# Optimization experiments

Measured on AMD Instinct MI355X. Metric: run time of the kernel, lower is better.

The kernel has to match this reference:

```python
import jax, jax.numpy as jnp
import numpy as np

TEMPERATURE = 0.5
BATCH = 2048  # N = batch_size * world_size (world_size = 1)
FEAT = 128
EPS = 1e-8  # torch CosineSimilarity default eps


def _build_mask_indices(N):
    """Replicates mask_correlated_samples + the row-major boolean gather
    sim[mask].reshape(2N, -1). Returns static flat indices [2N, 2N-1]."""
    sub = np.ones((2 * N, 2 * N), dtype=bool)
    np.fill_diagonal(sub, False)
    idx = np.arange(N)
    sub[idx, N + idx] = False
    sub[N + idx, idx] = False
    mask = np.zeros((3 * N, 3 * N), dtype=bool)
    mask[:2 * N, :2 * N] = sub
    mask[idx, 2 * N + idx] = True
    mask[2 * N + idx, idx] = True
    flat = np.nonzero(mask.ravel())[0]  # row-major order, 2N*(2N-1) entries
    return flat.reshape(2 * N, 2 * N - 1)


_NEG_IDX = jnp.asarray(_build_mask_indices(BATCH), dtype=jnp.int32)


def setup_inputs() -> dict:
    key = jax.random.key(0)
    ka, kp, kn = jax.random.split(key, 3)
    return {
        "anchor": jax.random.normal(ka, (BATCH, FEAT), dtype=jnp.float32),
        "pos": jax.random.normal(kp, (BATCH, FEAT), dtype=jnp.float32),
        "neg": jax.random.normal(kn, (BATCH, FEAT), dtype=jnp.float32),
    }


def reference(anchor, pos, neg):
    N = anchor.shape[0]
    z = jnp.concatenate([anchor, pos, neg], axis=0)  # [3N, d]
    zn = z / jnp.maximum(jnp.linalg.norm(z, axis=1, keepdims=True), EPS)
    sim = (zn @ zn.T) / TEMPERATURE  # [3N, 3N]
    # positive pairs: diagonals at offset +/-2N (anchor<->neg pairs)
    sim_i_j = jnp.diagonal(sim, offset=2 * N)[:N]
    sim_j_i = jnp.diagonal(sim, offset=-2 * N)[:N]
    positive = jnp.concatenate([sim_i_j, sim_j_i]).reshape(2 * N, 1)
    # masked gather of negatives (static index table, row-major order)
    negative = jnp.take(sim.ravel(), _NEG_IDX)  # [2N, 2N-1]
    logits = jnp.concatenate([positive, negative], axis=1)  # [2N, 2N]
    # cross-entropy with label 0, reduction='sum', then / (2N)
    loss = jnp.sum(jax.nn.logsumexp(logits, axis=1) - logits[:, 0]) / (2 * N)
    return loss
```

## Files before the change

### kernel.cpp

```cpp
#include <hip/hip_runtime.h>
#include <hip/hip_bf16.h>

#define N_      2048
#define TWO_N   4096
#define DFEAT   128
#define SCALE   2.0f
#define BROWS   128
#define BCOLS   128
#define NT      (BCOLS / 16)
#define LDSTR   136

typedef __attribute__((ext_vector_type(8))) short bf16x8;
typedef __attribute__((ext_vector_type(4))) float f32x4;

__global__ __launch_bounds__(256) void k_prep(const float* __restrict__ a,
                                              const float* __restrict__ p,
                                              const float* __restrict__ ng,
                                              __hip_bfloat16* __restrict__ zn16,
                                              float* __restrict__ dvec,
                                              float* __restrict__ accS,
                                              float* __restrict__ accP) {
  const int wave = threadIdx.x >> 6;
  const int lane = threadIdx.x & 63;
  const int row  = blockIdx.x * 4 + wave;

  if (threadIdx.x < 4)        accS[blockIdx.x * 4 + threadIdx.x] = 0.0f;
  else if (threadIdx.x < 6)   accP[blockIdx.x * 2 + threadIdx.x - 4] = 0.0f;

  if (row < N_) {
    float2 u = ((const float2*)(a  + (size_t)row * DFEAT))[lane];
    float2 w = ((const float2*)(ng + (size_t)row * DFEAT))[lane];
    float saa = u.x * u.x + u.y * u.y;
    float snn = w.x * w.x + w.y * w.y;
    float san = u.x * w.x + u.y * w.y;
#pragma unroll
    for (int m = 1; m < 64; m <<= 1) {
      saa += __shfl_xor(saa, m);
      snn += __shfl_xor(snn, m);
      san += __shfl_xor(san, m);
    }
    float na = fmaxf(sqrtf(saa), 1e-8f);
    float rn = 1.0f / na;
    __hip_bfloat162 h;
    h.x = __float2bfloat16(u.x * rn);
    h.y = __float2bfloat16(u.y * rn);
    ((__hip_bfloat162*)zn16)[row * (DFEAT / 2) + lane] = h;
    if (lane == 0)
      dvec[row] = SCALE * san / (na * fmaxf(sqrtf(snn), 1e-8f));
  } else {
    float2 v = ((const float2*)(p + (size_t)(row - N_) * DFEAT))[lane];
    float ss = v.x * v.x + v.y * v.y;
#pragma unroll
    for (int m = 1; m < 64; m <<= 1) ss += __shfl_xor(ss, m);
    float rn = 1.0f / fmaxf(sqrtf(ss), 1e-8f);
    __hip_bfloat162 h;
    h.x = __float2bfloat16(v.x * rn);
    h.y = __float2bfloat16(v.y * rn);
    ((__hip_bfloat162*)zn16)[row * (DFEAT / 2) + lane] = h;
  }
}

__global__ __launch_bounds__(256) void k_simsum(const __hip_bfloat16* __restrict__ zn16,
                                                float* __restrict__ accS,
                                                float* __restrict__ accP) {
  __shared__ short Bp[BCOLS * LDSTR];

  const int wave = threadIdx.x >> 6;
  const int lane = threadIdx.x & 63;
  const int lr   = lane & 15;
  const int kg   = lane >> 4;
  const int rows_base = blockIdx.x * BROWS + wave * 32;
  const int cb0 = blockIdx.y * BCOLS;
  const short* zs = (const short*)zn16;

  bf16x8 a0[4], a1[4];
#pragma unroll
  for (int kk = 0; kk < 4; ++kk) {
    a0[kk] = *(const bf16x8*)(zs + (size_t)(rows_base + lr) * DFEAT + kk * 32 + kg * 8);
    a1[kk] = *(const bf16x8*)(zs + (size_t)(rows_base + 16 + lr) * DFEAT + kk * 32 + kg * 8);
  }

#pragma unroll
  for (int it = 0; it < 8; ++it) {
    const int g   = it * 256 + threadIdx.x;
    const int col = g >> 4;
    const int q   = g & 15;
    bf16x8 v = *(const bf16x8*)(zs + (size_t)(cb0 + col) * DFEAT + q * 8);
    *(bf16x8*)(&Bp[col * LDSTR + q * 8]) = v;
  }
  __syncthreads();

  const bool hi = (rows_base >= N_);
  int rrow[2][4], prt[2][4];
#pragma unroll
  for (int t = 0; t < 2; ++t)
#pragma unroll
    for (int j = 0; j < 4; ++j) {
      rrow[t][j] = rows_base + t * 16 + kg * 4 + j;
      prt[t][j]  = hi ? (rrow[t][j] - N_) : (rrow[t][j] + N_);
    }

  float accPv[2][4] = {{0.f,0.f,0.f,0.f},{0.f,0.f,0.f,0.f}};
  float accSv[2][4] = {{0.f,0.f,0.f,0.f},{0.f,0.f,0.f,0.f}};

#pragma unroll 1
  for (int ct = 0; ct < NT; ++ct) {
    bf16x8 b[4];
#pragma unroll
    for (int kk = 0; kk < 4; ++kk)
      b[kk] = *(const bf16x8*)(&Bp[(ct * 16 + lr) * LDSTR + kk * 32 + kg * 8]);

    f32x4 acc0 = {0.f, 0.f, 0.f, 0.f};
    f32x4 acc1 = {0.f, 0.f, 0.f, 0.f};
#pragma unroll
    for (int kk = 0; kk < 4; ++kk) {
      acc0 = __builtin_amdgcn_mfma_f32_16x16x32_bf16(a0[kk], b[kk], acc0, 0, 0, 0);
      acc1 = __builtin_amdgcn_mfma_f32_16x16x32_bf16(a1[kk], b[kk], acc1, 0, 0, 0);
    }

    const int c = cb0 + ct * 16 + lr;
#pragma unroll
    for (int j = 0; j < 4; ++j) {
      {
        float e = __expf(SCALE * acc0[j]);
        const bool excl = (c == rrow[0][j]) || (c == prt[0][j]);
        e = excl ? 0.0f : e;
        if (hi) {
          const bool toP = (c < prt[0][j]);
          accPv[0][j] += toP ? e : 0.0f;
          accSv[0][j] += toP ? 0.0f : e;
        } else {
          accSv[0][j] += e;
        }
      }
      {
        float e = __expf(SCALE * acc1[j]);
        const bool excl = (c == rrow[1][j]) || (c == prt[1][j]);
        e = excl ? 0.0f : e;
        if (hi) {
          const bool toP = (c < prt[1][j]);
          accPv[1][j] += toP ? e : 0.0f;
          accSv[1][j] += toP ? 0.0f : e;
        } else {
          accSv[1][j] += e;
        }
      }
    }
  }

#pragma unroll
  for (int t = 0; t < 2; ++t)
#pragma unroll
    for (int j = 0; j < 4; ++j) {
      float pv = accPv[t][j], sv = accSv[t][j];
#pragma unroll
      for (int m = 1; m < 16; m <<= 1) {
        sv += __shfl_xor(sv, m);
        if (hi) pv += __shfl_xor(pv, m);
      }
      if (lr == 0) {
        atomicAdd(&accS[rrow[t][j]], sv);
        if (hi) atomicAdd(&accP[rrow[t][j] - N_], pv);
      }
    }
}

__global__ __launch_bounds__(1024) void k_final(const float* __restrict__ dvec,
                                                const float* __restrict__ accS,
                                                const float* __restrict__ accP,
                                                float* __restrict__ out) {
  __shared__ float Elds[N_];
  __shared__ float red[16];
  const int tid = threadIdx.x;
  float dpart = 0.f;
  for (int i = tid; i < N_; i += 1024) {
    float E = __expf(dvec[i]);
    Elds[i] = E;
    dpart += E;
  }
#pragma unroll
  for (int m = 1; m < 64; m <<= 1) dpart += __shfl_xor(dpart, m);
  const int w = tid >> 6, l = tid & 63;
  if (l == 0) red[w] = dpart;
  __syncthreads();
  float Dsum = 0.f;
#pragma unroll
  for (int k = 0; k < 16; ++k) Dsum += red[k];
  __syncthreads();

  float part = 0.f;
  for (int r = tid; r < TWO_N; r += 1024) {
    float S = accS[r];
    float t;
    if (r < N_) {
      t = logf(2.0f * Elds[r] + S) - dvec[r];
    } else {
      const int i = r - N_;
      const float extra = (i < N_ - 1) ? accP[i + 1] : Dsum;
      t = logf(Elds[i] + S + extra) - dvec[i];
    }
    part += t;
  }
#pragma unroll
  for (int m = 1; m < 64; m <<= 1) part += __shfl_xor(part, m);
  if (l == 0) red[w] = part;
  __syncthreads();
  if (tid == 0) {
    float tot = 0.f;
#pragma unroll
    for (int k = 0; k < 16; ++k) tot += red[k];
    out[0] = tot / (float)TWO_N;
  }
}

extern "C" void kernel_launch(void* const* d_in, const int* in_sizes, int n_in,
                              void* d_out, int out_size, void* d_ws, size_t ws_size,
                              hipStream_t stream) {
  const float* a  = (const float*)d_in[0];
  const float* p  = (const float*)d_in[1];
  const float* ng = (const float*)d_in[2];

  char* ws = (char*)d_ws;
  __hip_bfloat16* zn16 = (__hip_bfloat16*)ws;
  float* dvec = (float*)(ws + (size_t)TWO_N * DFEAT * 2);
  float* accS = dvec + TWO_N;
  float* accP = accS + TWO_N;

  k_prep<<<TWO_N / 4, 256, 0, stream>>>(a, p, ng, zn16, dvec, accS, accP);
  k_simsum<<<dim3(TWO_N / BROWS, TWO_N / BCOLS), 256, 0, stream>>>(zn16, accS, accP);
  k_final<<<1, 1024, 0, stream>>>(dvec, accS, accP, (float*)d_out);
}
```

Before: 26.79 us.

## Exploit similarity-matrix symmetry to compute only upper-triangular tiles in simsum

Blocks below the diagonal now return early, and each upper-triangle tile adds its exp values into both row sums and column sums using column reductions and atomics. The partner-block and accP split logic is re-derived for the transposed contributions. This roughly halves the MFMA and exp work in the dominant kernel. In exchange it adds per-tile cross-lane shuffles and many more atomics, launches idle blocks, and leaves the workload unbalanced.

```diff
diff --git a/kernel.cpp b/kernel.cpp
--- a/kernel.cpp
+++ b/kernel.cpp
@@ -63,15 +63,23 @@
 __global__ __launch_bounds__(256) void k_simsum(const __hip_bfloat16* __restrict__ zn16,
                                                 float* __restrict__ accS,
                                                 float* __restrict__ accP) {
+  const int bx = blockIdx.x, by = blockIdx.y;
+  if (by < bx) return;
+
   __shared__ short Bp[BCOLS * LDSTR];
 
   const int wave = threadIdx.x >> 6;
   const int lane = threadIdx.x & 63;
   const int lr   = lane & 15;
   const int kg   = lane >> 4;
-  const int rows_base = blockIdx.x * BROWS + wave * 32;
-  const int cb0 = blockIdx.y * BCOLS;
+  const int rb0  = bx * BROWS;
+  const int cb0  = by * BCOLS;
+  const int rows_base = rb0 + wave * 32;
   const short* zs = (const short*)zn16;
+
+  const bool isDiag    = (bx == by);
+  const bool isPartner = (by == bx + 16);
+  const bool colP      = (by >= 16) && (bx < by - 16);
 
   bf16x8 a0[4], a1[4];
 #pragma unroll
@@ -90,18 +98,9 @@
   }
   __syncthreads();
 
-  const bool hi = (rows_base >= N_);
-  int rrow[2][4], prt[2][4];
-#pragma unroll
-  for (int t = 0; t < 2; ++t)
-#pragma unroll
-    for (int j = 0; j < 4; ++j) {
-      rrow[t][j] = rows_base + t * 16 + kg * 4 + j;
-      prt[t][j]  = hi ? (rrow[t][j] - N_) : (rrow[t][j] + N_);
-    }
-
-  float accPv[2][4] = {{0.f,0.f,0.f,0.f},{0.f,0.f,0.f,0.f}};
-  float accSv[2][4] = {{0.f,0.f,0.f,0.f},{0.f,0.f,0.f,0.f}};
+  float rowS[2][4] = {{0.f,0.f,0.f,0.f},{0.f,0.f,0.f,0.f}};
+  const int r0base = rows_base + kg * 4;
+  const int r1base = rows_base + 16 + kg * 4;
 
 #pragma unroll 1
   for (int ct = 0; ct < NT; ++ct) {
@@ -118,33 +117,43 @@
       acc1 = __builtin_amdgcn_mfma_f32_16x16x32_bf16(a1[kk], b[kk], acc1, 0, 0, 0);
     }
 
-    const int c = cb0 + ct * 16 + lr;
+    const int c  = cb0 + ct * 16 + lr;
+    const int qc = c - N_;
+    float colv = 0.f, colvP = 0.f;
+
 #pragma unroll
     for (int j = 0; j < 4; ++j) {
-      {
-        float e = __expf(SCALE * acc0[j]);
-        const bool excl = (c == rrow[0][j]) || (c == prt[0][j]);
-        e = excl ? 0.0f : e;
-        if (hi) {
-          const bool toP = (c < prt[0][j]);
-          accPv[0][j] += toP ? e : 0.0f;
-          accSv[0][j] += toP ? 0.0f : e;
-        } else {
-          accSv[0][j] += e;
+      const int r0 = r0base + j;
+      float e0 = __expf(SCALE * acc0[j]);
+      if (isDiag)    e0 = (c  == r0) ? 0.0f : e0;
+      if (isPartner) e0 = (qc == r0) ? 0.0f : e0;
+      rowS[0][j] += e0;
+      if (isPartner) { if (r0 < qc) colvP += e0; else colv += e0; }
+      else colv += e0;
+
+      const int r1 = r1base + j;
+      float e1 = __expf(SCALE * acc1[j]);
+      if (isDiag)    e1 = (c  == r1) ? 0.0f : e1;
+      if (isPartner) e1 = (qc == r1) ? 0.0f : e1;
+      rowS[1][j] += e1;
+      if (isPartner) { if (r1 < qc) colvP += e1; else colv += e1; }
+      else colv += e1;
+    }
+
+    if (!isDiag) {
+      colv += __shfl_xor(colv, 16);
+      colv += __shfl_xor(colv, 32);
+      if (isPartner) {
+        colvP += __shfl_xor(colvP, 16);
+        colvP += __shfl_xor(colvP, 32);
+        if (kg == 0) {
+          atomicAdd(&accS[c], colv);
+          atomicAdd(&accP[qc], colvP);
         }
+      } else if (kg == 0) {
+        if (colP) atomicAdd(&accP[qc], colv);
+        else      atomicAdd(&accS[c],  colv);
       }
-      {
-        float e = __expf(SCALE * acc1[j]);
-        const bool excl = (c == rrow[1][j]) || (c == prt[1][j]);
-        e = excl ? 0.0f : e;
-        if (hi) {
-          const bool toP = (c < prt[1][j]);
-          accPv[1][j] += toP ? e : 0.0f;
-          accSv[1][j] += toP ? 0.0f : e;
-        } else {
-          accSv[1][j] += e;
-        }
-      }
     }
   }
 
@@ -152,16 +161,11 @@
   for (int t = 0; t < 2; ++t)
 #pragma unroll
     for (int j = 0; j < 4; ++j) {
-      float pv = accPv[t][j], sv = accSv[t][j];
-#pragma unroll
-      for (int m = 1; m < 16; m <<= 1) {
-        sv += __shfl_xor(sv, m);
-        if (hi) pv += __shfl_xor(pv, m);
-      }
-      if (lr == 0) {
-        atomicAdd(&accS[rrow[t][j]], sv);
-        if (hi) atomicAdd(&accP[rrow[t][j] - N_], pv);
-      }
+      float sv = rowS[t][j];
+#pragma unroll
+      for (int m = 1; m < 16; m <<= 1) sv += __shfl_xor(sv, m);
+      if (lr == 0)
+        atomicAdd(&accS[rows_base + t * 16 + kg * 4 + j], sv);
     }
 }
 
```

New measurement: 27.75 us. +3.6%, slower.
